# Kernel optimization log

Measured on AMD Instinct MI355X. Metric: run time of the kernel, lower is better.

## Reference

```python
import jax, jax.numpy as jnp
import numpy as np

ALPHA = 0.2  # LeakyReLU negative slope
MASK_FILL = -9e15


def setup_inputs() -> dict:
    key = jax.random.key(0)
    k_x, k_adj, k_W, k_a = jax.random.split(key, 4)
    B, N, Fin, T, O = 8, 1024, 64, 8, 128
    x = jax.random.normal(k_x, (B, N, Fin, T), dtype=jnp.float32)
    adj = (jax.random.uniform(k_adj, (N, N)) < 0.05).astype(jnp.float32)
    adj = jnp.maximum(adj, jnp.eye(N, dtype=jnp.float32))
    W = jax.random.normal(k_W, (Fin, O), dtype=jnp.float32) * (1.414 * (6.0 / (Fin + O)) ** 0.5)
    a = jax.random.normal(k_a, (2 * O, 1), dtype=jnp.float32) * (1.414 * (6.0 / (2 * O + 1)) ** 0.5)
    return {"x": x, "adj": adj, "W": W, "a": a}


def reference(x, adj, W, a):
    # x: (B, N, Fin, T), adj: (N, N), W: (Fin, O), a: (2O, 1)
    O = W.shape[1]
    xt = jnp.transpose(x, (0, 3, 1, 2))                 # (B, T, N, Fin)
    Wh = jnp.einsum('btnf,fo->btno', xt, W)             # (B, T, N, O)
    a1 = a[:O, 0]                                       # (O,)
    a2 = a[O:, 0]                                       # (O,)
    Wh1 = Wh @ a1                                       # (B, T, N)
    Wh2 = Wh @ a2                                       # (B, T, N)
    e = Wh1[..., :, None] + Wh2[..., None, :]           # (B, T, N, N): e_ij = Wh1_i + Wh2_j
    e = jax.nn.leaky_relu(e, negative_slope=ALPHA)
    e = jnp.where(adj > 0, e, MASK_FILL)
    attn = jax.nn.softmax(e, axis=-1)                   # softmax over neighbors j (torch dim=1 on (N,N))
    # dropout on attention is identity at inference (training=False)
    h_prime = jnp.einsum('btij,btjo->btio', attn, Wh)   # (B, T, N, O)
    out = jnp.transpose(h_prime, (0, 2, 3, 1))          # (B, N, O, T)
    return jax.nn.elu(out)                              # concat=True -> ELU
```

## Files before the change

kernel.cpp:

```cpp
#include <hip/hip_runtime.h>
#include <math.h>
#include <stdint.h>

#define ALPHA 0.2f

typedef __attribute__((ext_vector_type(8))) short bf16x8;
typedef __attribute__((ext_vector_type(4))) float f32x4;

__device__ __forceinline__ uint32_t pack_bf16(float a, float b) {
    return ((__float_as_uint(a) + 0x8000u) >> 16) |
           ((__float_as_uint(b) + 0x8000u) & 0xFFFF0000u);
}

__global__ __launch_bounds__(512, 4) void k_wh(const float* __restrict__ x,
                                               const float* __restrict__ W,
                                               const float* __restrict__ a,
                                               uint4* __restrict__ Whf,
                                               float* __restrict__ Wh1,
                                               float* __restrict__ Wh2) {
    __shared__ float xs[16 * 512];
    __shared__ float Wv[128 * 68];

    const int tid = threadIdx.x;
    const int b   = blockIdx.x & 7;
    const int jt  = blockIdx.x >> 3;

    const float4* xg4 = (const float4*)(x + (size_t)(b * 1024 + jt * 16) * 512);
    #pragma unroll
    for (int i = 0; i < 4; ++i) {
        int    idx = tid + i * 512;
        float4 v   = xg4[idx];
        int jl  = idx >> 7;
        int rem = idx & 127;
        int f   = rem >> 1;
        int tq  = rem & 1;
        int kk  = f ^ ((jl >> 2) << 2);
        float* dst = &xs[jl * 512 + (tq * 4) * 64 + kk];
        dst[0]   = v.x;
        dst[64]  = v.y;
        dst[128] = v.z;
        dst[192] = v.w;
    }
    const float4* Wg4 = (const float4*)W;
    #pragma unroll
    for (int i = 0; i < 4; ++i) {
        int    idx = tid + i * 512;
        float4 v   = Wg4[idx];
        int k  = idx >> 5;
        int o0 = (idx & 31) * 4;
        #pragma unroll
        for (int c = 0; c < 4; ++c) {
            int o   = o0 + c;
            int adr = o * 68 + ((((k >> 2) ^ ((o >> 3) & 7)) << 2) | (k & 3));
            Wv[adr] = (&v.x)[c];
        }
    }
    __syncthreads();

    const int w  = tid >> 6;
    const int l  = tid & 63;
    const int q  = l >> 4;
    const int om = l & 15;
    const int t  = w;

    float acc[4][8];
    #pragma unroll
    for (int jj = 0; jj < 4; ++jj)
        #pragma unroll
        for (int nt = 0; nt < 8; ++nt) acc[jj][nt] = 0.f;

    for (int kc = 0; kc < 64; kc += 4) {
        float4 xv[4], wv[8];
        const int kx = kc ^ (q << 2);
        #pragma unroll
        for (int jj = 0; jj < 4; ++jj)
            xv[jj] = *(const float4*)&xs[(q * 4 + jj) * 512 + t * 64 + kx];
        #pragma unroll
        for (int nt = 0; nt < 8; ++nt) {
            int og  = nt * 16 + om;
            int grp = (kc >> 2) ^ ((nt * 2 + (om >> 3)) & 7);
            wv[nt]  = *(const float4*)&Wv[og * 68 + grp * 4];
        }
        #pragma unroll
        for (int jj = 0; jj < 4; ++jj) {
            #pragma unroll
            for (int nt = 0; nt < 8; ++nt) {
                float s = acc[jj][nt];
                s = fmaf(xv[jj].x, wv[nt].x, s);
                s = fmaf(xv[jj].y, wv[nt].y, s);
                s = fmaf(xv[jj].z, wv[nt].z, s);
                s = fmaf(xv[jj].w, wv[nt].w, s);
                acc[jj][nt] = s;
            }
        }
    }

    const int bt = b * 8 + t;

    float a1v[8], a2v[8];
    #pragma unroll
    for (int nt = 0; nt < 8; ++nt) {
        a1v[nt] = a[nt * 16 + om];
        a2v[nt] = a[128 + nt * 16 + om];
    }
    #pragma unroll
    for (int jj = 0; jj < 4; ++jj) {
        float s1 = 0.f, s2 = 0.f;
        #pragma unroll
        for (int nt = 0; nt < 8; ++nt) {
            s1 = fmaf(acc[jj][nt], a1v[nt], s1);
            s2 = fmaf(acc[jj][nt], a2v[nt], s2);
        }
        #pragma unroll
        for (int off = 1; off < 16; off <<= 1) {
            s1 += __shfl_xor(s1, off);
            s2 += __shfl_xor(s2, off);
        }
        if (om == 0) {
            int j = jt * 16 + q * 4 + jj;
            Wh1[bt * 1024 + j] = s1;
            Wh2[bt * 1024 + j] = s2;
        }
    }

    const int    q8l   = ((jt & 1) << 1) | (q >> 1);
    const int    l8    = (q8l << 4) | om;
    const size_t fbase = (size_t)(bt * 32 + (jt >> 1)) * 8;
    #pragma unroll
    for (int nt = 0; nt < 8; ++nt) {
        uint2 st;
        st.x = pack_bf16(acc[0][nt], acc[1][nt]);
        st.y = pack_bf16(acc[2][nt], acc[3][nt]);
        char* p = (char*)(Whf + (fbase + nt) * 64 + l8) + ((q & 1) << 3);
        *(uint2*)p = st;
    }
}

__global__ __launch_bounds__(256) void k_adjb(const float* __restrict__ adj,
                                              unsigned char* __restrict__ adjb) {
    int idx = blockIdx.x * 256 + threadIdx.x;
    const float4* a4 = (const float4*)adj + idx * 2;
    float4 v0 = a4[0], v1 = a4[1];
    unsigned int by = 0;
    by |= (v0.x > 0.f) ? 1u : 0u;
    by |= (v0.y > 0.f) ? 2u : 0u;
    by |= (v0.z > 0.f) ? 4u : 0u;
    by |= (v0.w > 0.f) ? 8u : 0u;
    by |= (v1.x > 0.f) ? 16u : 0u;
    by |= (v1.y > 0.f) ? 32u : 0u;
    by |= (v1.z > 0.f) ? 64u : 0u;
    by |= (v1.w > 0.f) ? 128u : 0u;
    adjb[idx] = (unsigned char)by;
}

__global__ __launch_bounds__(512, 4) void k_agg(const uint4* __restrict__ Whf,
                                                const float* __restrict__ Wh1,
                                                const float* __restrict__ Wh2,
                                                const unsigned char* __restrict__ adjb,
                                                float* __restrict__ out) {
    __shared__ __attribute__((aligned(16))) float2 efs[1024];
    __shared__ unsigned int adjs_u[128 * 33];
    __shared__ float wh1s[128];
    __shared__ float m2s[8];

    const int tid   = threadIdx.x;
    const int b     = blockIdx.x & 7;
    const int t     = (blockIdx.x >> 3) & 7;
    const int itile = blockIdx.x >> 6;
    const int bt    = b * 8 + t;
    const int i0    = itile * 128;

    const int w = tid >> 6;
    const int l = tid & 63;
    const int q = l >> 4;
    const int m = l & 15;

    const float* wh2g = Wh2 + bt * 1024;
    float mx = -1e30f;
    for (int j = tid; j < 1024; j += 512) {
        float h2 = wh2g[j];
        float2 ef;
        ef.x = __expf(h2);
        ef.y = __expf(ALPHA * h2);
        efs[j] = ef;
        mx = fmaxf(mx, h2);
    }
    #pragma unroll
    for (int off = 1; off < 64; off <<= 1) mx = fmaxf(mx, __shfl_xor(mx, off));
    if (l == 0) m2s[w] = mx;
    if (tid < 128) wh1s[tid] = Wh1[bt * 1024 + i0 + tid];
    const unsigned int* adjg = (const unsigned int*)(adjb + i0 * 128);
    for (int idx = tid; idx < 4096; idx += 512)
        adjs_u[(idx >> 5) * 33 + (idx & 31)] = adjg[idx];
    __syncthreads();

    float M2 = m2s[0];
    #pragma unroll
    for (int i = 1; i < 8; ++i) M2 = fmaxf(M2, m2s[i]);

    const int   row = w * 16 + m;
    const float h1  = wh1s[row];
    const float e0  = h1 + M2;
    const float mp  = fmaxf(e0, ALPHA * e0);
    const float Af  = __expf(h1 - mp);
    const float Bf  = __expf(ALPHA * h1 - mp);
    const float G   = __expf(-h1);

    f32x4 acc[8];
    #pragma unroll
    for (int nt = 0; nt < 8; ++nt) acc[nt] = (f32x4){0.f, 0.f, 0.f, 0.f};
    f32x4 accl = (f32x4){0.f, 0.f, 0.f, 0.f};

    bf16x8 ones;
    #pragma unroll
    for (int i = 0; i < 8; ++i) ones[i] = (short)0x3F80;

    const uint4* bfg = Whf + (size_t)bt * 32 * 8 * 64 + l;

    for (int s = 0; s < 32; ++s) {
        const float* eb = (const float*)&efs[s * 32 + q * 8];
        float4 ef01 = *(const float4*)(eb + 0);
        float4 ef23 = *(const float4*)(eb + 4);
        float4 ef45 = *(const float4*)(eb + 8);
        float4 ef67 = *(const float4*)(eb + 12);
        const unsigned int dw = adjs_u[row * 33 + s];

        float E[8], F[8];
        E[0] = ef01.x; F[0] = ef01.y; E[1] = ef01.z; F[1] = ef01.w;
        E[2] = ef23.x; F[2] = ef23.y; E[3] = ef23.z; F[3] = ef23.w;
        E[4] = ef45.x; F[4] = ef45.y; E[5] = ef45.z; F[5] = ef45.w;
        E[6] = ef67.x; F[6] = ef67.y; E[7] = ef67.z; F[7] = ef67.w;

        float p[8];
        #pragma unroll
        for (int jj = 0; jj < 8; ++jj) {
            bool  cond = E[jj] > G;
            float pr   = (cond ? Af : Bf) * (cond ? E[jj] : F[jj]);
            p[jj] = ((dw >> (q * 8 + jj)) & 1u) ? pr : 0.0f;
        }

        union { uint32_t u[4]; bf16x8 v; } pk;
        #pragma unroll
        for (int pr2 = 0; pr2 < 4; ++pr2)
            pk.u[pr2] = pack_bf16(p[2 * pr2], p[2 * pr2 + 1]);

        const uint4* bp = bfg + (size_t)s * 8 * 64;
        #pragma unroll
        for (int nt = 0; nt < 8; ++nt) {
            union { uint4 u; bf16x8 v; } br;
            br.u = bp[nt * 64];
            acc[nt] = __builtin_amdgcn_mfma_f32_16x16x32_bf16(pk.v, br.v, acc[nt], 0, 0, 0);
        }
        accl = __builtin_amdgcn_mfma_f32_16x16x32_bf16(pk.v, ones, accl, 0, 0, 0);
    }

    float* og = out + ((size_t)(b * 1024 + i0 + w * 16)) * 1024 + t;
    #pragma unroll
    for (int reg = 0; reg < 4; ++reg) {
        const int   r    = q * 4 + reg;
        const float linv = 1.0f / accl[reg];
        #pragma unroll
        for (int nt = 0; nt < 8; ++nt) {
            float v = acc[nt][reg] * linv;
            v = v > 0.f ? v : __expf(v) - 1.f;
            og[(size_t)r * 1024 + (nt * 16 + m) * 8] = v;
        }
    }
}

extern "C" void kernel_launch(void* const* d_in, const int* in_sizes, int n_in,
                              void* d_out, int out_size, void* d_ws, size_t ws_size,
                              hipStream_t stream) {
    const float* x   = (const float*)d_in[0];
    const float* adj = (const float*)d_in[1];
    const float* W   = (const float*)d_in[2];
    const float* a   = (const float*)d_in[3];
    float* out = (float*)d_out;

    uint4*         Whf  = (uint4*)d_ws;
    float*         Wh1  = (float*)(Whf + 1048576);
    float*         Wh2  = Wh1 + 65536;
    unsigned char* adjb = (unsigned char*)(Wh2 + 65536);

    k_wh  <<<512, 512, 0, stream>>>(x, W, a, Whf, Wh1, Wh2);
    k_adjb<<<512, 256, 0, stream>>>(adj, adjb);
    k_agg <<<512, 512, 0, stream>>>(Whf, Wh1, Wh2, adjb, out);
}
```

Baseline: 159.8 us.

## Stage Wh B-tiles in shared memory and give each wave two row tiles

The aggregation kernel drops to 256 threads per block, and each wave now computes two 16-row M tiles. Both tiles share each B fragment, which now comes from a double-buffered LDS stage filled by register prefetch from global memory, instead of every wave reading global memory directly. The aim is to cut redundant global/L2 traffic for Wh and hide load latency. In exchange it adds a __syncthreads per step and roughly doubles accumulator registers. The k_wh occupancy hint is also relaxed.

```diff
diff --git a/kernel.cpp b/kernel.cpp
--- a/kernel.cpp
+++ b/kernel.cpp
@@ -12,12 +12,12 @@
            ((__float_as_uint(b) + 0x8000u) & 0xFFFF0000u);
 }
 
-__global__ __launch_bounds__(512, 4) void k_wh(const float* __restrict__ x,
-                                               const float* __restrict__ W,
-                                               const float* __restrict__ a,
-                                               uint4* __restrict__ Whf,
-                                               float* __restrict__ Wh1,
-                                               float* __restrict__ Wh2) {
+__global__ __launch_bounds__(512) void k_wh(const float* __restrict__ x,
+                                            const float* __restrict__ W,
+                                            const float* __restrict__ a,
+                                            uint4* __restrict__ Whf,
+                                            float* __restrict__ Wh1,
+                                            float* __restrict__ Wh2) {
     __shared__ float xs[16 * 512];
     __shared__ float Wv[128 * 68];
 
@@ -153,15 +153,16 @@
     adjb[idx] = (unsigned char)by;
 }
 
-__global__ __launch_bounds__(512, 4) void k_agg(const uint4* __restrict__ Whf,
+__global__ __launch_bounds__(256, 2) void k_agg(const uint4* __restrict__ Whf,
                                                 const float* __restrict__ Wh1,
                                                 const float* __restrict__ Wh2,
                                                 const unsigned char* __restrict__ adjb,
                                                 float* __restrict__ out) {
+    __shared__ __attribute__((aligned(16))) uint4  bstage[2][512];
     __shared__ __attribute__((aligned(16))) float2 efs[1024];
     __shared__ unsigned int adjs_u[128 * 33];
     __shared__ float wh1s[128];
-    __shared__ float m2s[8];
+    __shared__ float m2s[4];
 
     const int tid   = threadIdx.x;
     const int b     = blockIdx.x & 7;
@@ -175,9 +176,14 @@
     const int q = l >> 4;
     const int m = l & 15;
 
+    const uint4* plane = Whf + (size_t)bt * 16384;
+
+    uint4 pf0 = plane[tid];
+    uint4 pf1 = plane[256 + tid];
+
     const float* wh2g = Wh2 + bt * 1024;
     float mx = -1e30f;
-    for (int j = tid; j < 1024; j += 512) {
+    for (int j = tid; j < 1024; j += 256) {
         float h2 = wh2g[j];
         float2 ef;
         ef.x = __expf(h2);
@@ -190,80 +196,107 @@
     if (l == 0) m2s[w] = mx;
     if (tid < 128) wh1s[tid] = Wh1[bt * 1024 + i0 + tid];
     const unsigned int* adjg = (const unsigned int*)(adjb + i0 * 128);
-    for (int idx = tid; idx < 4096; idx += 512)
+    for (int idx = tid; idx < 4096; idx += 256)
         adjs_u[(idx >> 5) * 33 + (idx & 31)] = adjg[idx];
+
+    bstage[0][tid]       = pf0;
+    bstage[0][tid + 256] = pf1;
     __syncthreads();
 
-    float M2 = m2s[0];
-    #pragma unroll
-    for (int i = 1; i < 8; ++i) M2 = fmaxf(M2, m2s[i]);
-
-    const int   row = w * 16 + m;
-    const float h1  = wh1s[row];
-    const float e0  = h1 + M2;
-    const float mp  = fmaxf(e0, ALPHA * e0);
-    const float Af  = __expf(h1 - mp);
-    const float Bf  = __expf(ALPHA * h1 - mp);
-    const float G   = __expf(-h1);
-
-    f32x4 acc[8];
-    #pragma unroll
-    for (int nt = 0; nt < 8; ++nt) acc[nt] = (f32x4){0.f, 0.f, 0.f, 0.f};
-    f32x4 accl = (f32x4){0.f, 0.f, 0.f, 0.f};
+    float M2 = fmaxf(fmaxf(m2s[0], m2s[1]), fmaxf(m2s[2], m2s[3]));
+
+    float h1v[2], Af[2], Bf[2], G[2];
+    int   arow[2];
+    #pragma unroll
+    for (int ms = 0; ms < 2; ++ms) {
+        int   row = w * 32 + ms * 16 + m;
+        float h1  = wh1s[row];
+        float e0  = h1 + M2;
+        float mp  = fmaxf(e0, ALPHA * e0);
+        h1v[ms]  = h1;
+        Af[ms]   = __expf(h1 - mp);
+        Bf[ms]   = __expf(ALPHA * h1 - mp);
+        G[ms]    = __expf(-h1);
+        arow[ms] = row * 33;
+    }
+
+    f32x4 acc[2][8];
+    #pragma unroll
+    for (int ms = 0; ms < 2; ++ms)
+        #pragma unroll
+        for (int nt = 0; nt < 8; ++nt) acc[ms][nt] = (f32x4){0.f, 0.f, 0.f, 0.f};
+    f32x4 accl[2] = {(f32x4){0.f, 0.f, 0.f, 0.f}, (f32x4){0.f, 0.f, 0.f, 0.f}};
 
     bf16x8 ones;
     #pragma unroll
     for (int i = 0; i < 8; ++i) ones[i] = (short)0x3F80;
 
-    const uint4* bfg = Whf + (size_t)bt * 32 * 8 * 64 + l;
-
     for (int s = 0; s < 32; ++s) {
+        if (s + 1 < 32) {
+            pf0 = plane[(s + 1) * 512 + tid];
+            pf1 = plane[(s + 1) * 512 + 256 + tid];
+        }
+
         const float* eb = (const float*)&efs[s * 32 + q * 8];
         float4 ef01 = *(const float4*)(eb + 0);
         float4 ef23 = *(const float4*)(eb + 4);
         float4 ef45 = *(const float4*)(eb + 8);
         float4 ef67 = *(const float4*)(eb + 12);
-        const unsigned int dw = adjs_u[row * 33 + s];
-
         float E[8], F[8];
         E[0] = ef01.x; F[0] = ef01.y; E[1] = ef01.z; F[1] = ef01.w;
         E[2] = ef23.x; F[2] = ef23.y; E[3] = ef23.z; F[3] = ef23.w;
         E[4] = ef45.x; F[4] = ef45.y; E[5] = ef45.z; F[5] = ef45.w;
         E[6] = ef67.x; F[6] = ef67.y; E[7] = ef67.z; F[7] = ef67.w;
 
-        float p[8];
-        #pragma unroll
-        for (int jj = 0; jj < 8; ++jj) {
-            bool  cond = E[jj] > G;
-            float pr   = (cond ? Af : Bf) * (cond ? E[jj] : F[jj]);
-            p[jj] = ((dw >> (q * 8 + jj)) & 1u) ? pr : 0.0f;
-        }
-
-        union { uint32_t u[4]; bf16x8 v; } pk;
-        #pragma unroll
-        for (int pr2 = 0; pr2 < 4; ++pr2)
-            pk.u[pr2] = pack_bf16(p[2 * pr2], p[2 * pr2 + 1]);
-
-        const uint4* bp = bfg + (size_t)s * 8 * 64;
+        bf16x8 afr[2];
+        #pragma unroll
+        for (int ms = 0; ms < 2; ++ms) {
+            const unsigned int dw = adjs_u[arow[ms] + s];
+            float p[8];
+            #pragma unroll
+            for (int jj = 0; jj < 8; ++jj) {
+                bool  cond = E[jj] > G[ms];
+                float pr   = (cond ? Af[ms] : Bf[ms]) * (cond ? E[jj] : F[jj]);
+                p[jj] = ((dw >> (q * 8 + jj)) & 1u) ? pr : 0.0f;
+            }
+            union { uint32_t u[4]; bf16x8 v; } pk;
+            #pragma unroll
+            for (int pr2 = 0; pr2 < 4; ++pr2)
+                pk.u[pr2] = pack_bf16(p[2 * pr2], p[2 * pr2 + 1]);
+            afr[ms] = pk.v;
+        }
+
+        const uint4* bp = &bstage[s & 1][l];
         #pragma unroll
         for (int nt = 0; nt < 8; ++nt) {
             union { uint4 u; bf16x8 v; } br;
             br.u = bp[nt * 64];
-            acc[nt] = __builtin_amdgcn_mfma_f32_16x16x32_bf16(pk.v, br.v, acc[nt], 0, 0, 0);
-        }
-        accl = __builtin_amdgcn_mfma_f32_16x16x32_bf16(pk.v, ones, accl, 0, 0, 0);
-    }
-
-    float* og = out + ((size_t)(b * 1024 + i0 + w * 16)) * 1024 + t;
-    #pragma unroll
-    for (int reg = 0; reg < 4; ++reg) {
-        const int   r    = q * 4 + reg;
-        const float linv = 1.0f / accl[reg];
-        #pragma unroll
-        for (int nt = 0; nt < 8; ++nt) {
-            float v = acc[nt][reg] * linv;
-            v = v > 0.f ? v : __expf(v) - 1.f;
-            og[(size_t)r * 1024 + (nt * 16 + m) * 8] = v;
+            acc[0][nt] = __builtin_amdgcn_mfma_f32_16x16x32_bf16(afr[0], br.v, acc[0][nt], 0, 0, 0);
+            acc[1][nt] = __builtin_amdgcn_mfma_f32_16x16x32_bf16(afr[1], br.v, acc[1][nt], 0, 0, 0);
+        }
+        accl[0] = __builtin_amdgcn_mfma_f32_16x16x32_bf16(afr[0], ones, accl[0], 0, 0, 0);
+        accl[1] = __builtin_amdgcn_mfma_f32_16x16x32_bf16(afr[1], ones, accl[1], 0, 0, 0);
+
+        if (s + 1 < 32) {
+            bstage[(s + 1) & 1][tid]       = pf0;
+            bstage[(s + 1) & 1][tid + 256] = pf1;
+        }
+        __syncthreads();
+    }
+
+    #pragma unroll
+    for (int ms = 0; ms < 2; ++ms) {
+        float* og = out + ((size_t)(b * 1024 + i0 + w * 32 + ms * 16)) * 1024 + t;
+        #pragma unroll
+        for (int reg = 0; reg < 4; ++reg) {
+            const int   r    = q * 4 + reg;
+            const float linv = 1.0f / accl[ms][reg];
+            #pragma unroll
+            for (int nt = 0; nt < 8; ++nt) {
+                float v = acc[ms][nt][reg] * linv;
+                v = v > 0.f ? v : __expf(v) - 1.f;
+                og[(size_t)r * 1024 + (nt * 16 + m) * 8] = v;
+            }
         }
     }
 }
@@ -284,5 +317,5 @@
 
     k_wh  <<<512, 512, 0, stream>>>(x, W, a, Whf, Wh1, Wh2);
     k_adjb<<<512, 256, 0, stream>>>(adj, adjb);
-    k_agg <<<512, 512, 0, stream>>>(Whf, Wh1, Wh2, adjb, out);
-}
+    k_agg <<<512, 256, 0, stream>>>(Whf, Wh1, Wh2, adjb, out);
+}
```

Measured after the change: 152.2 us. 4.8% less time.

## Stage Wh B-tiles through double-buffered LDS with register prefetch; preload adjacency in registers

Applied to the files above, without the earlier changes.

The aggregation kernel now loads each 8 KB slab of the bf16 Wh fragment plane cooperatively, one uint4 per thread. Each slab is prefetched into a register one step ahead and stored into a double-buffered LDS stage, so every wave reads B operands from LDS instead of each wave fetching the same data from global memory. The adjacency bitmask is stored permuted so each thread can load its row's mask bytes directly into registers, replacing the padded shared-memory copy. In exchange, a __syncthreads is added per k-step, and k_wh loses its occupancy hint in launch_bounds.

```diff
diff --git a/kernel.cpp b/kernel.cpp
--- a/kernel.cpp
+++ b/kernel.cpp
@@ -12,12 +12,12 @@
            ((__float_as_uint(b) + 0x8000u) & 0xFFFF0000u);
 }
 
-__global__ __launch_bounds__(512, 4) void k_wh(const float* __restrict__ x,
-                                               const float* __restrict__ W,
-                                               const float* __restrict__ a,
-                                               uint4* __restrict__ Whf,
-                                               float* __restrict__ Wh1,
-                                               float* __restrict__ Wh2) {
+__global__ __launch_bounds__(512) void k_wh(const float* __restrict__ x,
+                                            const float* __restrict__ W,
+                                            const float* __restrict__ a,
+                                            uint4* __restrict__ Whf,
+                                            float* __restrict__ Wh1,
+                                            float* __restrict__ Wh2) {
     __shared__ float xs[16 * 512];
     __shared__ float Wv[128 * 68];
 
@@ -137,8 +137,10 @@
 }
 
 __global__ __launch_bounds__(256) void k_adjb(const float* __restrict__ adj,
-                                              unsigned char* __restrict__ adjb) {
+                                              unsigned char* __restrict__ adjq) {
     int idx = blockIdx.x * 256 + threadIdx.x;
+    int i   = idx >> 7;
+    int pos = idx & 127;
     const float4* a4 = (const float4*)adj + idx * 2;
     float4 v0 = a4[0], v1 = a4[1];
     unsigned int by = 0;
@@ -150,16 +152,16 @@
     by |= (v1.y > 0.f) ? 32u : 0u;
     by |= (v1.z > 0.f) ? 64u : 0u;
     by |= (v1.w > 0.f) ? 128u : 0u;
-    adjb[idx] = (unsigned char)by;
+    adjq[i * 128 + (pos & 3) * 32 + (pos >> 2)] = (unsigned char)by;
 }
 
 __global__ __launch_bounds__(512, 4) void k_agg(const uint4* __restrict__ Whf,
                                                 const float* __restrict__ Wh1,
                                                 const float* __restrict__ Wh2,
-                                                const unsigned char* __restrict__ adjb,
+                                                const unsigned char* __restrict__ adjq,
                                                 float* __restrict__ out) {
+    __shared__ __attribute__((aligned(16))) uint4  bstage[2][512];
     __shared__ __attribute__((aligned(16))) float2 efs[1024];
-    __shared__ unsigned int adjs_u[128 * 33];
     __shared__ float wh1s[128];
     __shared__ float m2s[8];
 
@@ -174,10 +176,20 @@
     const int l = tid & 63;
     const int q = l >> 4;
     const int m = l & 15;
+    const int row = w * 16 + m;
+
+    const uint4* plane = Whf + (size_t)bt * 16384;
+
+    uint4 pf = plane[tid];
+    const uint4* amask = (const uint4*)(adjq + (i0 + row) * 128 + q * 32);
+    uint4 adj0 = amask[0];
+    uint4 adj1 = amask[1];
 
     const float* wh2g = Wh2 + bt * 1024;
     float mx = -1e30f;
-    for (int j = tid; j < 1024; j += 512) {
+    #pragma unroll
+    for (int rep = 0; rep < 2; ++rep) {
+        int   j  = tid + rep * 512;
         float h2 = wh2g[j];
         float2 ef;
         ef.x = __expf(h2);
@@ -189,22 +201,20 @@
     for (int off = 1; off < 64; off <<= 1) mx = fmaxf(mx, __shfl_xor(mx, off));
     if (l == 0) m2s[w] = mx;
     if (tid < 128) wh1s[tid] = Wh1[bt * 1024 + i0 + tid];
-    const unsigned int* adjg = (const unsigned int*)(adjb + i0 * 128);
-    for (int idx = tid; idx < 4096; idx += 512)
-        adjs_u[(idx >> 5) * 33 + (idx & 31)] = adjg[idx];
+
+    bstage[0][tid] = pf;
     __syncthreads();
 
     float M2 = m2s[0];
     #pragma unroll
     for (int i = 1; i < 8; ++i) M2 = fmaxf(M2, m2s[i]);
 
-    const int   row = w * 16 + m;
-    const float h1  = wh1s[row];
-    const float e0  = h1 + M2;
-    const float mp  = fmaxf(e0, ALPHA * e0);
-    const float Af  = __expf(h1 - mp);
-    const float Bf  = __expf(ALPHA * h1 - mp);
-    const float G   = __expf(-h1);
+    const float h1 = wh1s[row];
+    const float e0 = h1 + M2;
+    const float mp = fmaxf(e0, ALPHA * e0);
+    const float Af = __expf(h1 - mp);
+    const float Bf = __expf(ALPHA * h1 - mp);
+    const float G  = __expf(-h1);
 
     f32x4 acc[8];
     #pragma unroll
@@ -215,36 +225,39 @@
     #pragma unroll
     for (int i = 0; i < 8; ++i) ones[i] = (short)0x3F80;
 
-    const uint4* bfg = Whf + (size_t)bt * 32 * 8 * 64 + l;
-
+    #pragma unroll
     for (int s = 0; s < 32; ++s) {
+        if (s + 1 < 32) pf = plane[(s + 1) * 512 + tid];
+
         const float* eb = (const float*)&efs[s * 32 + q * 8];
         float4 ef01 = *(const float4*)(eb + 0);
         float4 ef23 = *(const float4*)(eb + 4);
         float4 ef45 = *(const float4*)(eb + 8);
         float4 ef67 = *(const float4*)(eb + 12);
-        const unsigned int dw = adjs_u[row * 33 + s];
-
         float E[8], F[8];
         E[0] = ef01.x; F[0] = ef01.y; E[1] = ef01.z; F[1] = ef01.w;
         E[2] = ef23.x; F[2] = ef23.y; E[3] = ef23.z; F[3] = ef23.w;
         E[4] = ef45.x; F[4] = ef45.y; E[5] = ef45.z; F[5] = ef45.w;
         E[6] = ef67.x; F[6] = ef67.y; E[7] = ef67.z; F[7] = ef67.w;
 
+        const uint4   av = (s < 16) ? adj0 : adj1;
+        const int     c  = (s >> 2) & 3;
+        const uint32_t cw = (c == 0) ? av.x : (c == 1) ? av.y : (c == 2) ? av.z : av.w;
+        const uint32_t by = (cw >> ((s & 3) * 8)) & 0xFFu;
+
         float p[8];
         #pragma unroll
         for (int jj = 0; jj < 8; ++jj) {
             bool  cond = E[jj] > G;
             float pr   = (cond ? Af : Bf) * (cond ? E[jj] : F[jj]);
-            p[jj] = ((dw >> (q * 8 + jj)) & 1u) ? pr : 0.0f;
-        }
-
+            p[jj] = ((by >> jj) & 1u) ? pr : 0.0f;
+        }
         union { uint32_t u[4]; bf16x8 v; } pk;
         #pragma unroll
         for (int pr2 = 0; pr2 < 4; ++pr2)
             pk.u[pr2] = pack_bf16(p[2 * pr2], p[2 * pr2 + 1]);
 
-        const uint4* bp = bfg + (size_t)s * 8 * 64;
+        const uint4* bp = &bstage[s & 1][l];
         #pragma unroll
         for (int nt = 0; nt < 8; ++nt) {
             union { uint4 u; bf16x8 v; } br;
@@ -252,6 +265,9 @@
             acc[nt] = __builtin_amdgcn_mfma_f32_16x16x32_bf16(pk.v, br.v, acc[nt], 0, 0, 0);
         }
         accl = __builtin_amdgcn_mfma_f32_16x16x32_bf16(pk.v, ones, accl, 0, 0, 0);
+
+        if (s + 1 < 32) bstage[(s + 1) & 1][tid] = pf;
+        __syncthreads();
     }
 
     float* og = out + ((size_t)(b * 1024 + i0 + w * 16)) * 1024 + t;
@@ -280,9 +296,9 @@
     uint4*         Whf  = (uint4*)d_ws;
     float*         Wh1  = (float*)(Whf + 1048576);
     float*         Wh2  = Wh1 + 65536;
-    unsigned char* adjb = (unsigned char*)(Wh2 + 65536);
+    unsigned char* adjq = (unsigned char*)(Wh2 + 65536);
 
     k_wh  <<<512, 512, 0, stream>>>(x, W, a, Whf, Wh1, Wh2);
-    k_adjb<<<512, 256, 0, stream>>>(adj, adjb);
-    k_agg <<<512, 512, 0, stream>>>(Whf, Wh1, Wh2, adjb, out);
-}
+    k_adjb<<<512, 256, 0, stream>>>(adj, adjq);
+    k_agg <<<512, 512, 0, stream>>>(Whf, Wh1, Wh2, adjq, out);
+}
```

Result: faster. 147.3 us (-7.9%).
